# Kernel optimization log

Measured on AMD Instinct MI355X. Metric: run time of the kernel, lower is better.

The kernel has to match this reference:

```python
import jax, jax.numpy as jnp
import numpy as np

EOS_ID = 2
PAD_ID = 0


def setup_inputs() -> dict:
    key = jax.random.key(0)
    ks = jax.random.split(key, 10)
    B, E, H, V, T = 64, 512, 512, 32000, 20
    features = jax.random.normal(ks[0], (B, E), dtype=jnp.float32)
    captions = jax.random.randint(ks[1], (B, T), 0, V)            # unused in policy branch
    lengths = jax.random.randint(ks[2], (B,), 1, T + 1)
    lengths = lengths.at[0].set(T)                                 # make max(lengths) == 20 deterministic
    # parameters (match torch init scales roughly)
    embed_W = jax.random.uniform(ks[3], (V, E), jnp.float32, -0.1, 0.1)
    s = 1.0 / np.sqrt(H)
    W_ih = jax.random.uniform(ks[4], (4 * H, E), jnp.float32, -s, s)
    W_hh = jax.random.uniform(ks[5], (4 * H, H), jnp.float32, -s, s)
    b_ih = jax.random.uniform(ks[6], (4 * H,), jnp.float32, -s, s)
    b_hh = jax.random.uniform(ks[7], (4 * H,), jnp.float32, -s, s)
    linear_W = jax.random.uniform(ks[8], (V, H), jnp.float32, -0.1, 0.1)
    linear_b = jnp.zeros((V,), jnp.float32)
    return {"features": features, "captions": captions, "lengths": lengths,
            "use_policy": 1, "embed_W": embed_W, "W_ih": W_ih, "W_hh": W_hh,
            "b_ih": b_ih, "b_hh": b_hh, "linear_W": linear_W, "linear_b": linear_b}


def _lstm_cell(x, h, c, W_ih, W_hh, b_ih, b_hh):
    # PyTorch gate order: i, f, g, o
    gates = x @ W_ih.T + b_ih + h @ W_hh.T + b_hh        # [B, 4H]
    i, f, g, o = jnp.split(gates, 4, axis=-1)
    i, f, o = jax.nn.sigmoid(i), jax.nn.sigmoid(f), jax.nn.sigmoid(o)
    g = jnp.tanh(g)
    c = f * c + i * g
    h = o * jnp.tanh(c)
    return h, c


def reference(features, captions, lengths, use_policy, embed_W, W_ih, W_hh,
              b_ih, b_hh, linear_W, linear_b):
    # LSTM decode with categorical sampling, stopping per-example at EOS (id 2)
    # and padding remaining steps with id 0 / log_prob 0. The original loops
    # over batch and time with batch-size-1 kernels; here we batch + lax.scan.
    B, H = features.shape[0], W_hh.shape[1]
    T = int(jnp.max(lengths))                            # concrete at trace setup
    step_keys = jax.random.split(jax.random.key(42), T)

    def step(carry, key_t):
        h, c, x, done = carry
        h, c = _lstm_cell(x, h, c, W_ih, W_hh, b_ih, b_hh)
        logits = h @ linear_W.T + linear_b               # [B, V]
        logp = jax.nn.log_softmax(logits, axis=-1)
        tok = jax.random.categorical(key_t, logits)      # [B] int32
        lp = jnp.take_along_axis(logp, tok[:, None], axis=1)[:, 0]
        ids_rec = jnp.where(done, PAD_ID, tok)
        lp_rec = jnp.where(done, 0.0, lp)
        done = done | ((tok == EOS_ID) & ~done)          # EOS token itself is recorded
        x = embed_W[tok]                                 # next-step input embedding
        return (h, c, x, done), (ids_rec, lp_rec)

    init = (jnp.zeros((B, H), features.dtype), jnp.zeros((B, H), features.dtype),
            features, jnp.zeros((B,), bool))
    _, (ids, logps) = jax.lax.scan(step, init, step_keys)
    sampled_ids = jnp.transpose(ids)                     # [B, T]
    saved_log_probs = jnp.transpose(logps)               # [B, T]
    return sampled_ids, saved_log_probs
```

## Files before the change

### kernel.cpp

```cpp
#include <hip/hip_runtime.h>
#include <hip/hip_bf16.h>
#include <stdint.h>
#include <float.h>

#define BB 64
#define EE 512
#define HH 512
#define VV 32000
#define TT 20
#define INV2048 0.00048828125f

typedef _Float16 f16x8 __attribute__((ext_vector_type(8)));
typedef float f32x4 __attribute__((ext_vector_type(4)));

__device__ __host__ __forceinline__ void tf2x32(uint32_t k0, uint32_t k1, uint32_t x0, uint32_t x1,
                                                uint32_t& o0, uint32_t& o1) {
  const uint32_t k2 = k0 ^ k1 ^ 0x1BD11BDAu;
  x0 += k0; x1 += k1;
#define RND(R) { x0 += x1; x1 = (x1 << R) | (x1 >> (32 - R)); x1 ^= x0; }
  RND(13) RND(15) RND(26) RND(6)
  x0 += k1; x1 += k2 + 1u;
  RND(17) RND(29) RND(16) RND(24)
  x0 += k2; x1 += k0 + 2u;
  RND(13) RND(15) RND(26) RND(6)
  x0 += k0; x1 += k1 + 3u;
  RND(17) RND(29) RND(16) RND(24)
  x0 += k1; x1 += k2 + 4u;
  RND(13) RND(15) RND(26) RND(6)
  x0 += k2; x1 += k0 + 5u;
#undef RND
  o0 = x0; o1 = x1;
}

__device__ __forceinline__ float gumbel_for(uint32_t k1t, uint32_t k2t, uint32_t idx) {
  uint32_t o0, o1; tf2x32(k1t, k2t, 0u, idx, o0, o1);
  uint32_t bits = o0 ^ o1;
  uint32_t mant = bits >> 9;
  float f = __uint_as_float(0x3f800000u | mant) - 1.0f;
  float u = mant ? f : 1.1754943508222875e-38f;
  return -logf(-logf(u));
}

struct Part { float bv; int bix; float blog; float m; float s; };

__device__ __forceinline__ void part_combine(Part& P, const Part& Q) {
  if (Q.bv > P.bv || (Q.bv == P.bv && Q.bix < P.bix)) { P.bv = Q.bv; P.bix = Q.bix; P.blog = Q.blog; }
  if (Q.m > P.m) { P.s = P.s * expf(P.m - Q.m) + Q.s; P.m = Q.m; }
  else           { P.s += Q.s * expf(Q.m - P.m); }
}

__global__ __launch_bounds__(256) void k_init(float* __restrict__ hA, float* __restrict__ cT,
                                              int* __restrict__ done) {
  int i = blockIdx.x * 256 + threadIdx.x;
  if (i < HH * BB) { hA[i] = 0.f; cT[i] = 0.f; }
  if (i < BB) done[i] = 0;
}

__global__ __launch_bounds__(256) void k_gates(const float* __restrict__ xin,
                                               const float* __restrict__ hT,
                                               const float* __restrict__ Wih,
                                               const float* __restrict__ Whh,
                                               float* __restrict__ gatesP) {
  const int jt = blockIdx.x;
  const int kc = blockIdx.y;
  const int tx = threadIdx.x;
  __shared__ float a[64][64];
  __shared__ float wj[64][68];
  const int bi = (tx & 15) * 4;
  const int ji = (tx >> 4) * 4;
  float acc[4][4] = {};
  const float* Wsrc = (kc < 4) ? Wih : Whh;
  for (int s = 0; s < 2; ++s) {
    const int kg = kc * 128 + s * 64;
    if (kc < 4) {
      #pragma unroll
      for (int r = 0; r < 4; ++r) {
        int fi = r * 256 + tx;
        int b = fi >> 4, k4 = (fi & 15) * 4;
        const float4 v = *(const float4*)(xin + b * EE + kg + k4);
        a[k4 + 0][b] = v.x; a[k4 + 1][b] = v.y; a[k4 + 2][b] = v.z; a[k4 + 3][b] = v.w;
      }
    } else {
      #pragma unroll
      for (int r = 0; r < 4; ++r) {
        int fi = r * 256 + tx;
        int row = fi >> 4, c4 = (fi & 15) * 4;
        *(float4*)(&a[row][c4]) = *(const float4*)(hT + (kg - 512 + row) * BB + c4);
      }
    }
    const int kcol = kg & 511;
    #pragma unroll
    for (int r = 0; r < 4; ++r) {
      int fi = r * 256 + tx;
      int j = fi >> 4, k4 = (fi & 15) * 4;
      const float4 v = *(const float4*)(Wsrc + (size_t)(jt * 64 + j) * EE + kcol + k4);
      wj[k4 + 0][j] = v.x; wj[k4 + 1][j] = v.y; wj[k4 + 2][j] = v.z; wj[k4 + 3][j] = v.w;
    }
    __syncthreads();
    #pragma unroll 8
    for (int kk = 0; kk < 64; ++kk) {
      const float4 av = *(const float4*)(&a[kk][bi]);
      const float4 wv = *(const float4*)(&wj[kk][ji]);
      const float avx[4] = {av.x, av.y, av.z, av.w};
      const float wvx[4] = {wv.x, wv.y, wv.z, wv.w};
      #pragma unroll
      for (int jj = 0; jj < 4; ++jj)
        #pragma unroll
        for (int bb = 0; bb < 4; ++bb)
          acc[jj][bb] = fmaf(wvx[jj], avx[bb], acc[jj][bb]);
    }
    __syncthreads();
  }
  #pragma unroll
  for (int jj = 0; jj < 4; ++jj) {
    float4 o = make_float4(acc[jj][0], acc[jj][1], acc[jj][2], acc[jj][3]);
    *(float4*)(gatesP + ((size_t)kc * 2048 + jt * 64 + ji + jj) * BB + bi) = o;
  }
}

__global__ __launch_bounds__(256) void k_lstm_update(const float* __restrict__ gatesP,
                                                     const float* __restrict__ b_ih,
                                                     const float* __restrict__ b_hh,
                                                     float* __restrict__ cT,
                                                     float* __restrict__ hT) {
  const int blk = blockIdx.x;
  const int tx = threadIdx.x;
  const int b = tx & 63;
  const int dk = tx >> 6;
  #pragma unroll
  for (int r = 0; r < 2; ++r) {
    const int k = blk * 8 + dk + r * 4;
    float g[4];
    #pragma unroll
    for (int gi = 0; gi < 4; ++gi) {
      const int j = gi * 512 + k;
      float s = 0.f;
      #pragma unroll
      for (int kc = 0; kc < 8; ++kc) s += gatesP[((size_t)kc * 2048 + j) * BB + b];
      g[gi] = s + b_ih[j] + b_hh[j];
    }
    const float ig = 1.f / (1.f + expf(-g[0]));
    const float fg = 1.f / (1.f + expf(-g[1]));
    const float gg = tanhf(g[2]);
    const float og = 1.f / (1.f + expf(-g[3]));
    const float c = fg * cT[k * BB + b] + ig * gg;
    cT[k * BB + b] = c;
    hT[k * BB + b] = og * tanhf(c);
  }
}

__global__ __launch_bounds__(256) void k_lstm_update_frag(const float* __restrict__ gatesP,
                                                          const float* __restrict__ b_ih,
                                                          const float* __restrict__ b_hh,
                                                          float* __restrict__ cT,
                                                          float* __restrict__ hT,
                                                          _Float16* __restrict__ hfh,
                                                          _Float16* __restrict__ hfl) {
  const int blk = blockIdx.x;
  const int tx = threadIdx.x;
  const int b = tx & 63;
  const int dk = tx >> 6;
  #pragma unroll
  for (int r = 0; r < 2; ++r) {
    const int k = blk * 8 + dk + r * 4;
    float g[4];
    #pragma unroll
    for (int gi = 0; gi < 4; ++gi) {
      const int j = gi * 512 + k;
      float s = 0.f;
      #pragma unroll
      for (int kc = 0; kc < 8; ++kc) s += gatesP[((size_t)kc * 2048 + j) * BB + b];
      g[gi] = s + b_ih[j] + b_hh[j];
    }
    const float ig = 1.f / (1.f + expf(-g[0]));
    const float fg = 1.f / (1.f + expf(-g[1]));
    const float gg = tanhf(g[2]);
    const float og = 1.f / (1.f + expf(-g[3]));
    const float c = fg * cT[k * BB + b] + ig * gg;
    cT[k * BB + b] = c;
    const float h = og * tanhf(c);
    hT[k * BB + b] = h;
    const _Float16 hh = (_Float16)h;
    const _Float16 hl = (_Float16)((h - (float)hh) * 2048.0f);
    const int cc = k >> 5, kr = k & 31;
    const int lane = (kr >> 3) * 16 + (b & 15), j = kr & 7, nb = b >> 4;
    const int idx = ((cc * 4 + nb) * 64 + lane) * 8 + j;
    hfh[idx] = hh; hfl[idx] = hl;
  }
}

__global__ __launch_bounds__(256) void k_convW2(const float* __restrict__ LW,
                                                _Float16* __restrict__ Wh,
                                                _Float16* __restrict__ Wl) {
  const int bv = blockIdx.x, bk = blockIdx.y;
  const int tx = threadIdx.x;
  __shared__ float lds[64][65];
  #pragma unroll
  for (int r = 0; r < 4; ++r) {
    const int fi = r * 256 + tx;
    const int vl = fi >> 4, k4 = (fi & 15) * 4;
    const float4 v = *(const float4*)(LW + (size_t)(bv * 64 + vl) * HH + bk * 64 + k4);
    lds[vl][k4] = v.x; lds[vl][k4 + 1] = v.y; lds[vl][k4 + 2] = v.z; lds[vl][k4 + 3] = v.w;
  }
  __syncthreads();
  #pragma unroll
  for (int r = 0; r < 2; ++r) {
    const int u = r * 256 + tx;
    const int frag = u >> 6;
    const int vbl = frag >> 1, cl = frag & 1;
    const int lane = u & 63;
    const int m = lane & 15, lh = lane >> 4;
    f16x8 hi, lo;
    #pragma unroll
    for (int j = 0; j < 8; ++j) {
      const float f = lds[vbl * 16 + m][cl * 32 + lh * 8 + j];
      const _Float16 h = (_Float16)f;
      hi[j] = h;
      lo[j] = (_Float16)((f - (float)h) * 2048.0f);
    }
    const size_t o = (((size_t)(bv * 4 + vbl) * 16 + (bk * 2 + cl)) * 64 + lane) * 8;
    *(f16x8*)(Wh + o) = hi;
    *(f16x8*)(Wl + o) = lo;
  }
}

__global__ __launch_bounds__(256) void k_logits4(const f16x8* __restrict__ Wh,
                                                 const f16x8* __restrict__ Wl,
                                                 const f16x8* __restrict__ hfh,
                                                 const f16x8* __restrict__ hfl,
                                                 const float* __restrict__ lb,
                                                 uint32_t k1t, uint32_t k2t,
                                                 float4* __restrict__ pf4,
                                                 int* __restrict__ pidx) {
  const int wv = threadIdx.x >> 6;
  const int vt = blockIdx.x * 4 + wv;
  const int lane = threadIdx.x & 63;
  __shared__ float red[4][64][5];
  const f32x4 zero = {0.f, 0.f, 0.f, 0.f};
  f32x4 aH[4]  = {zero, zero, zero, zero};
  f32x4 aM1[4] = {zero, zero, zero, zero};
  f32x4 aM2[4] = {zero, zero, zero, zero};
  const size_t wbase = (size_t)vt * 16 * 64 + lane;
  f16x8 whC = Wh[wbase], wlC = Wl[wbase];
  #pragma unroll 4
  for (int c = 0; c < 16; ++c) {
    f16x8 whN, wlN;
    if (c < 15) { whN = Wh[wbase + (c + 1) * 64]; wlN = Wl[wbase + (c + 1) * 64]; }
    #pragma unroll
    for (int nb = 0; nb < 4; ++nb) {
      const f16x8 bh = hfh[(c * 4 + nb) * 64 + lane];
      const f16x8 bl = hfl[(c * 4 + nb) * 64 + lane];
      aH[nb]  = __builtin_amdgcn_mfma_f32_16x16x32_f16(whC, bh, aH[nb], 0, 0, 0);
      aM1[nb] = __builtin_amdgcn_mfma_f32_16x16x32_f16(whC, bl, aM1[nb], 0, 0, 0);
      aM2[nb] = __builtin_amdgcn_mfma_f32_16x16x32_f16(wlC, bh, aM2[nb], 0, 0, 0);
    }
    whC = whN; wlC = wlN;
  }
  const int v0 = vt * 16 + ((lane >> 4) << 2);
  const float4 bias = *(const float4*)(lb + v0);
  const float bb4[4] = {bias.x, bias.y, bias.z, bias.w};
  Part P[4];
  #pragma unroll
  for (int nb = 0; nb < 4; ++nb) {
    const int b = nb * 16 + (lane & 15);
    float lg = aH[nb][0] + (aM1[nb][0] + aM2[nb][0]) * INV2048 + bb4[0];
    Part p;
    p.bv = lg + gumbel_for(k1t, k2t, (uint32_t)(b * VV + v0));
    p.bix = v0; p.blog = lg; p.m = lg; p.s = 1.0f;
    #pragma unroll
    for (int reg = 1; reg < 4; ++reg) {
      float lg2 = aH[nb][reg] + (aM1[nb][reg] + aM2[nb][reg]) * INV2048 + bb4[reg];
      float pe = lg2 + gumbel_for(k1t, k2t, (uint32_t)(b * VV + v0 + reg));
      if (pe > p.bv) { p.bv = pe; p.bix = v0 + reg; p.blog = lg2; }
      if (lg2 > p.m) { p.s = p.s * expf(p.m - lg2) + 1.f; p.m = lg2; }
      else           { p.s += expf(lg2 - p.m); }
    }
    P[nb] = p;
  }
  #pragma unroll
  for (int msk = 16; msk <= 32; msk <<= 1) {
    #pragma unroll
    for (int nb = 0; nb < 4; ++nb) {
      Part Q;
      Q.bv   = __shfl_xor(P[nb].bv, msk, 64);
      Q.bix  = __shfl_xor(P[nb].bix, msk, 64);
      Q.blog = __shfl_xor(P[nb].blog, msk, 64);
      Q.m    = __shfl_xor(P[nb].m, msk, 64);
      Q.s    = __shfl_xor(P[nb].s, msk, 64);
      part_combine(P[nb], Q);
    }
  }
  if (lane < 16) {
    #pragma unroll
    for (int nb = 0; nb < 4; ++nb) {
      const int b = nb * 16 + lane;
      red[wv][b][0] = P[nb].bv; red[wv][b][1] = __int_as_float(P[nb].bix);
      red[wv][b][2] = P[nb].blog; red[wv][b][3] = P[nb].m; red[wv][b][4] = P[nb].s;
    }
  }
  __syncthreads();
  if (threadIdx.x < 64) {
    const int b = threadIdx.x;
    Part Pc;
    Pc.bv = red[0][b][0]; Pc.bix = __float_as_int(red[0][b][1]); Pc.blog = red[0][b][2];
    Pc.m = red[0][b][3]; Pc.s = red[0][b][4];
    #pragma unroll
    for (int w = 1; w < 4; ++w) {
      Part Q;
      Q.bv = red[w][b][0]; Q.bix = __float_as_int(red[w][b][1]); Q.blog = red[w][b][2];
      Q.m = red[w][b][3]; Q.s = red[w][b][4];
      part_combine(Pc, Q);
    }
    pf4[(size_t)blockIdx.x * BB + b] = make_float4(Pc.bv, Pc.blog, Pc.m, Pc.s);
    pidx[blockIdx.x * BB + b] = Pc.bix;
  }
}

__global__ __launch_bounds__(128) void k_logits2(const float* __restrict__ hT,
                                                 const float* __restrict__ LW,
                                                 const float* __restrict__ lb,
                                                 uint32_t k1t, uint32_t k2t,
                                                 float4* __restrict__ pf4,
                                                 int* __restrict__ pidx) {
  const int vt = blockIdx.x;
  const int tx = threadIdx.x;
  __shared__ float lds[5120];
  float* wTs = lds;
  const int vthr = tx & 15;
  const int bthr = tx >> 4;
  const int vi = vthr * 2;
  const int bi = bthr * 8;
  const int vq = tx >> 4;
  const int ks = tx & 15;
  float acc[2][8] = {};
  for (int kt = 0; kt < 8; ++kt) {
    const int kg = kt * 64;
    #pragma unroll
    for (int s = 0; s < 4; ++s) {
      const int kk = ks + 16 * s;
      const size_t rb = (size_t)(vt * 32 + 4 * vq) * HH + kg + kk;
      float w0 = LW[rb];
      float w1 = LW[rb + HH];
      float w2 = LW[rb + 2 * HH];
      float w3 = LW[rb + 3 * HH];
      const int ph = (4 * vq) ^ (4 * (kk & 7));
      *(float4*)&wTs[kk * 32 + ph] = make_float4(w0, w1, w2, w3);
    }
    __syncthreads();
    #pragma unroll 4
    for (int kk = 0; kk < 64; ++kk) {
      const float* hrow = hT + (size_t)(kg + kk) * BB;
      const float4 h0 = *(const float4*)(hrow + bi);
      const float4 h1 = *(const float4*)(hrow + bi + 4);
      const float2 wv = *(const float2*)&wTs[kk * 32 + (vi ^ (4 * (kk & 7)))];
      acc[0][0] = fmaf(wv.x, h0.x, acc[0][0]); acc[0][1] = fmaf(wv.x, h0.y, acc[0][1]);
      acc[0][2] = fmaf(wv.x, h0.z, acc[0][2]); acc[0][3] = fmaf(wv.x, h0.w, acc[0][3]);
      acc[0][4] = fmaf(wv.x, h1.x, acc[0][4]); acc[0][5] = fmaf(wv.x, h1.y, acc[0][5]);
      acc[0][6] = fmaf(wv.x, h1.z, acc[0][6]); acc[0][7] = fmaf(wv.x, h1.w, acc[0][7]);
      acc[1][0] = fmaf(wv.y, h0.x, acc[1][0]); acc[1][1] = fmaf(wv.y, h0.y, acc[1][1]);
      acc[1][2] = fmaf(wv.y, h0.z, acc[1][2]); acc[1][3] = fmaf(wv.y, h0.w, acc[1][3]);
      acc[1][4] = fmaf(wv.y, h1.x, acc[1][4]); acc[1][5] = fmaf(wv.y, h1.y, acc[1][5]);
      acc[1][6] = fmaf(wv.y, h1.z, acc[1][6]); acc[1][7] = fmaf(wv.y, h1.w, acc[1][7]);
    }
    __syncthreads();
  }
  const int v0g = vt * 32 + vi;
  const float bias0 = lb[v0g];
  const float bias1 = lb[v0g + 1];
  float* red = lds;
  #pragma unroll
  for (int bb = 0; bb < 8; ++bb) {
    const int b = bi + bb;
    const float lg0 = acc[0][bb] + bias0;
    const float lg1 = acc[1][bb] + bias1;
    Part p;
    p.bv = lg0 + gumbel_for(k1t, k2t, (uint32_t)(b * VV + v0g));
    p.bix = v0g; p.blog = lg0;
    const float pe1 = lg1 + gumbel_for(k1t, k2t, (uint32_t)(b * VV + v0g + 1));
    if (pe1 > p.bv) { p.bv = pe1; p.bix = v0g + 1; p.blog = lg1; }
    if (lg0 >= lg1) { p.m = lg0; p.s = 1.f + expf(lg1 - lg0); }
    else            { p.m = lg1; p.s = 1.f + expf(lg0 - lg1); }
    const int slot = (b * 16 + vthr) * 5;
    red[slot + 0] = p.bv; red[slot + 1] = __int_as_float(p.bix); red[slot + 2] = p.blog;
    red[slot + 3] = p.m;  red[slot + 4] = p.s;
  }
  __syncthreads();
  if (tx < 64) {
    const int b = tx;
    Part P;
    { const int s0 = (b * 16) * 5;
      P.bv = red[s0]; P.bix = __float_as_int(red[s0 + 1]); P.blog = red[s0 + 2];
      P.m = red[s0 + 3]; P.s = red[s0 + 4]; }
    #pragma unroll
    for (int c = 1; c < 16; ++c) {
      const int s0 = (b * 16 + c) * 5;
      Part Q; Q.bv = red[s0]; Q.bix = __float_as_int(red[s0 + 1]); Q.blog = red[s0 + 2];
      Q.m = red[s0 + 3]; Q.s = red[s0 + 4];
      part_combine(P, Q);
    }
    pf4[(size_t)vt * BB + b] = make_float4(P.bv, P.blog, P.m, P.s);
    pidx[vt * BB + b] = P.bix;
  }
}

__global__ __launch_bounds__(256) void k_sample2(const float4* __restrict__ pf4,
                                                 const int* __restrict__ pidx,
                                                 const float* __restrict__ embW,
                                                 int* __restrict__ done,
                                                 float* __restrict__ x,
                                                 float* __restrict__ out,
                                                 int step, int nvt) {
  const int b = blockIdx.x;
  const int tx = threadIdx.x;
  __shared__ float red[256 * 5];
  __shared__ int stok;
  Part p; p.bv = -FLT_MAX; p.bix = 0x7fffffff; p.blog = 0.f; p.m = -FLT_MAX; p.s = 0.f;
  for (int vt = tx; vt < nvt; vt += 256) {
    float4 q = pf4[(size_t)vt * BB + b];
    Part Q; Q.bv = q.x; Q.blog = q.y; Q.m = q.z; Q.s = q.w; Q.bix = pidx[vt * BB + b];
    part_combine(p, Q);
  }
  red[tx * 5 + 0] = p.bv; red[tx * 5 + 1] = __int_as_float(p.bix); red[tx * 5 + 2] = p.blog;
  red[tx * 5 + 3] = p.m;  red[tx * 5 + 4] = p.s;
  __syncthreads();
  for (int st = 128; st > 0; st >>= 1) {
    if (tx < st) {
      const int s0 = tx * 5, s1 = (tx + st) * 5;
      Part P, Q;
      P.bv = red[s0]; P.bix = __float_as_int(red[s0 + 1]); P.blog = red[s0 + 2]; P.m = red[s0 + 3]; P.s = red[s0 + 4];
      Q.bv = red[s1]; Q.bix = __float_as_int(red[s1 + 1]); Q.blog = red[s1 + 2]; Q.m = red[s1 + 3]; Q.s = red[s1 + 4];
      part_combine(P, Q);
      red[s0] = P.bv; red[s0 + 1] = __int_as_float(P.bix); red[s0 + 2] = P.blog; red[s0 + 3] = P.m; red[s0 + 4] = P.s;
    }
    __syncthreads();
  }
  if (tx == 0) {
    const int tok = __float_as_int(red[1]);
    const float blog = red[2], M = red[3], S = red[4];
    const float lp = blog - (M + logf(S));
    const int dn = done[b];
    out[b * TT + step] = dn ? 0.0f : (float)tok;
    out[BB * TT + b * TT + step] = dn ? 0.0f : lp;
    done[b] = dn | (tok == 2);
    stok = tok;
  }
  __syncthreads();
  const int tok = stok;
  for (int e = tx; e < EE; e += 256) x[b * EE + e] = embW[(size_t)tok * EE + e];
}

extern "C" void kernel_launch(void* const* d_in, const int* in_sizes, int n_in,
                              void* d_out, int out_size, void* d_ws, size_t ws_size,
                              hipStream_t stream) {
  const float* features = (const float*)d_in[0];
  const float* embW     = (const float*)d_in[4];
  const float* Wih      = (const float*)d_in[5];
  const float* Whh      = (const float*)d_in[6];
  const float* bih      = (const float*)d_in[7];
  const float* bhh      = (const float*)d_in[8];
  const float* LW       = (const float*)d_in[9];
  const float* lb       = (const float*)d_in[10];
  float* out = (float*)d_out;

  uint32_t keys[TT][2];
  for (int t = 0; t < TT; ++t) tf2x32(0u, 42u, 0u, (uint32_t)t, keys[t][0], keys[t][1]);

  float* ws = (float*)d_ws;
  float* hA = ws;
  float* hB = ws + 32768;
  float* cT = ws + 65536;
  float* x  = ws + 98304;

  if (ws_size >= (size_t)73000000) {
    float*  gatesP = ws + 131072;
    float4* pf4    = (float4*)(ws + 1179648);
    int*    pidx   = (int*)(ws + 1691648);
    int*    done   = (int*)(ws + 1819648);
    _Float16* hfh  = (_Float16*)(ws + 1819712);
    _Float16* hfl  = (_Float16*)(ws + 1836096);
    _Float16* Whi  = (_Float16*)(ws + 1852480);
    _Float16* Wlo  = (_Float16*)(ws + 10044480);

    k_convW2<<<dim3(500, 8), dim3(256), 0, stream>>>(LW, Whi, Wlo);
    k_init<<<dim3(128), dim3(256), 0, stream>>>(hA, cT, done);
    const float* hin = hA;
    float* hout = hB;
    for (int t = 0; t < TT; ++t) {
      const float* xin = (t == 0) ? features : x;
      k_gates<<<dim3(32, 8), dim3(256), 0, stream>>>(xin, hin, Wih, Whh, gatesP);
      k_lstm_update_frag<<<dim3(64), dim3(256), 0, stream>>>(gatesP, bih, bhh, cT, hout, hfh, hfl);
      k_logits4<<<dim3(500), dim3(256), 0, stream>>>((const f16x8*)Whi, (const f16x8*)Wlo,
                                                     (const f16x8*)hfh, (const f16x8*)hfl,
                                                     lb, keys[t][0], keys[t][1], pf4, pidx);
      k_sample2<<<dim3(64), dim3(256), 0, stream>>>(pf4, pidx, embW, done, x, out, t, 500);
      const float* tmp = hout; hout = (float*)hin; hin = tmp;
    }
  } else {
    float*  gatesP = ws + 131072;
    float4* pf4    = (float4*)(ws + 131072 + 1048576);
    int*    pidx   = (int*)(ws + 131072 + 1048576 + 256000);
    int*    done   = (int*)(ws + 131072 + 1048576 + 256000 + 64000);

    k_init<<<dim3(128), dim3(256), 0, stream>>>(hA, cT, done);
    const float* hin = hA;
    float* hout = hB;
    for (int t = 0; t < TT; ++t) {
      const float* xin = (t == 0) ? features : x;
      k_gates<<<dim3(32, 8), dim3(256), 0, stream>>>(xin, hin, Wih, Whh, gatesP);
      k_lstm_update<<<dim3(64), dim3(256), 0, stream>>>(gatesP, bih, bhh, cT, hout);
      k_logits2<<<dim3(1000), dim3(128), 0, stream>>>(hout, LW, lb, keys[t][0], keys[t][1], pf4, pidx);
      k_sample2<<<dim3(64), dim3(256), 0, stream>>>(pf4, pidx, embW, done, x, out, t, 1000);
      const float* tmp = hout; hout = (float*)hin; hin = tmp;
    }
  }
}
```

Before: 935.3 us.

## Fuse embedding gather into gates kernel and deepen logits prefetch pipeline

The sampling kernel now writes only the sampled token ids, and the gate GEMM kernel gathers embedding rows directly by token id. This removes the intermediate x buffer write and read on every step. The logits MFMA loop now prefetches weight fragments four chunks ahead and double-buffers the hidden-state fragments in registers, which is meant to hide global load latency. The cost is higher register pressure in the logits kernel and scattered row reads of the embedding table inside the gates kernel.

Result: slower. 1.051 ms (+12.4%).

```diff
diff --git a/kernel.cpp b/kernel.cpp
--- a/kernel.cpp
+++ b/kernel.cpp
@@ -56,20 +56,61 @@
   if (i < BB) done[i] = 0;
 }
 
-__global__ __launch_bounds__(256) void k_gates(const float* __restrict__ xin,
-                                               const float* __restrict__ hT,
-                                               const float* __restrict__ Wih,
-                                               const float* __restrict__ Whh,
-                                               float* __restrict__ gatesP) {
+__global__ __launch_bounds__(256) void k_convW2(const float* __restrict__ LW,
+                                                _Float16* __restrict__ Wh,
+                                                _Float16* __restrict__ Wl) {
+  const int bv = blockIdx.x, bk = blockIdx.y;
+  const int tx = threadIdx.x;
+  __shared__ float lds[64][65];
+  #pragma unroll
+  for (int r = 0; r < 4; ++r) {
+    const int fi = r * 256 + tx;
+    const int vl = fi >> 4, k4 = (fi & 15) * 4;
+    const float4 v = *(const float4*)(LW + (size_t)(bv * 64 + vl) * HH + bk * 64 + k4);
+    lds[vl][k4] = v.x; lds[vl][k4 + 1] = v.y; lds[vl][k4 + 2] = v.z; lds[vl][k4 + 3] = v.w;
+  }
+  __syncthreads();
+  #pragma unroll
+  for (int r = 0; r < 2; ++r) {
+    const int u = r * 256 + tx;
+    const int frag = u >> 6;
+    const int vbl = frag >> 1, cl = frag & 1;
+    const int lane = u & 63;
+    const int m = lane & 15, lh = lane >> 4;
+    f16x8 hi, lo;
+    #pragma unroll
+    for (int j = 0; j < 8; ++j) {
+      const float f = lds[vbl * 16 + m][cl * 32 + lh * 8 + j];
+      const _Float16 h = (_Float16)f;
+      hi[j] = h;
+      lo[j] = (_Float16)((f - (float)h) * 2048.0f);
+    }
+    const size_t o = (((size_t)(bv * 4 + vbl) * 16 + (bk * 2 + cl)) * 64 + lane) * 8;
+    *(f16x8*)(Wh + o) = hi;
+    *(f16x8*)(Wl + o) = lo;
+  }
+}
+
+__global__ __launch_bounds__(256) void k_gates2(const float* __restrict__ xin,
+                                                const float* __restrict__ embW,
+                                                const int* __restrict__ tok,
+                                                int use_tok,
+                                                const float* __restrict__ hT,
+                                                const float* __restrict__ Wih,
+                                                const float* __restrict__ Whh,
+                                                float* __restrict__ gatesP) {
   const int jt = blockIdx.x;
   const int kc = blockIdx.y;
   const int tx = threadIdx.x;
   __shared__ float a[64][64];
   __shared__ float wj[64][68];
+  __shared__ int ltok[64];
+  if (tx < 64) ltok[tx] = use_tok ? tok[tx] : 0;
   const int bi = (tx & 15) * 4;
   const int ji = (tx >> 4) * 4;
   float acc[4][4] = {};
   const float* Wsrc = (kc < 4) ? Wih : Whh;
+  __syncthreads();
   for (int s = 0; s < 2; ++s) {
     const int kg = kc * 128 + s * 64;
     if (kc < 4) {
@@ -77,7 +118,8 @@
       for (int r = 0; r < 4; ++r) {
         int fi = r * 256 + tx;
         int b = fi >> 4, k4 = (fi & 15) * 4;
-        const float4 v = *(const float4*)(xin + b * EE + kg + k4);
+        const float* rowsrc = use_tok ? (embW + (size_t)ltok[b] * EE) : (xin + (size_t)b * EE);
+        const float4 v = *(const float4*)(rowsrc + kg + k4);
         a[k4 + 0][b] = v.x; a[k4 + 1][b] = v.y; a[k4 + 2][b] = v.z; a[k4 + 3][b] = v.w;
       }
     } else {
@@ -115,37 +157,6 @@
   for (int jj = 0; jj < 4; ++jj) {
     float4 o = make_float4(acc[jj][0], acc[jj][1], acc[jj][2], acc[jj][3]);
     *(float4*)(gatesP + ((size_t)kc * 2048 + jt * 64 + ji + jj) * BB + bi) = o;
-  }
-}
-
-__global__ __launch_bounds__(256) void k_lstm_update(const float* __restrict__ gatesP,
-                                                     const float* __restrict__ b_ih,
-                                                     const float* __restrict__ b_hh,
-                                                     float* __restrict__ cT,
-                                                     float* __restrict__ hT) {
-  const int blk = blockIdx.x;
-  const int tx = threadIdx.x;
-  const int b = tx & 63;
-  const int dk = tx >> 6;
-  #pragma unroll
-  for (int r = 0; r < 2; ++r) {
-    const int k = blk * 8 + dk + r * 4;
-    float g[4];
-    #pragma unroll
-    for (int gi = 0; gi < 4; ++gi) {
-      const int j = gi * 512 + k;
-      float s = 0.f;
-      #pragma unroll
-      for (int kc = 0; kc < 8; ++kc) s += gatesP[((size_t)kc * 2048 + j) * BB + b];
-      g[gi] = s + b_ih[j] + b_hh[j];
-    }
-    const float ig = 1.f / (1.f + expf(-g[0]));
-    const float fg = 1.f / (1.f + expf(-g[1]));
-    const float gg = tanhf(g[2]);
-    const float og = 1.f / (1.f + expf(-g[3]));
-    const float c = fg * cT[k * BB + b] + ig * gg;
-    cT[k * BB + b] = c;
-    hT[k * BB + b] = og * tanhf(c);
   }
 }
 
@@ -189,42 +200,7 @@
   }
 }
 
-__global__ __launch_bounds__(256) void k_convW2(const float* __restrict__ LW,
-                                                _Float16* __restrict__ Wh,
-                                                _Float16* __restrict__ Wl) {
-  const int bv = blockIdx.x, bk = blockIdx.y;
-  const int tx = threadIdx.x;
-  __shared__ float lds[64][65];
-  #pragma unroll
-  for (int r = 0; r < 4; ++r) {
-    const int fi = r * 256 + tx;
-    const int vl = fi >> 4, k4 = (fi & 15) * 4;
-    const float4 v = *(const float4*)(LW + (size_t)(bv * 64 + vl) * HH + bk * 64 + k4);
-    lds[vl][k4] = v.x; lds[vl][k4 + 1] = v.y; lds[vl][k4 + 2] = v.z; lds[vl][k4 + 3] = v.w;
-  }
-  __syncthreads();
-  #pragma unroll
-  for (int r = 0; r < 2; ++r) {
-    const int u = r * 256 + tx;
-    const int frag = u >> 6;
-    const int vbl = frag >> 1, cl = frag & 1;
-    const int lane = u & 63;
-    const int m = lane & 15, lh = lane >> 4;
-    f16x8 hi, lo;
-    #pragma unroll
-    for (int j = 0; j < 8; ++j) {
-      const float f = lds[vbl * 16 + m][cl * 32 + lh * 8 + j];
-      const _Float16 h = (_Float16)f;
-      hi[j] = h;
-      lo[j] = (_Float16)((f - (float)h) * 2048.0f);
-    }
-    const size_t o = (((size_t)(bv * 4 + vbl) * 16 + (bk * 2 + cl)) * 64 + lane) * 8;
-    *(f16x8*)(Wh + o) = hi;
-    *(f16x8*)(Wl + o) = lo;
-  }
-}
-
-__global__ __launch_bounds__(256) void k_logits4(const f16x8* __restrict__ Wh,
+__global__ __launch_bounds__(256) void k_logits5(const f16x8* __restrict__ Wh,
                                                  const f16x8* __restrict__ Wl,
                                                  const f16x8* __restrict__ hfh,
                                                  const f16x8* __restrict__ hfl,
@@ -241,20 +217,32 @@
   f32x4 aM1[4] = {zero, zero, zero, zero};
   f32x4 aM2[4] = {zero, zero, zero, zero};
   const size_t wbase = (size_t)vt * 16 * 64 + lane;
-  f16x8 whC = Wh[wbase], wlC = Wl[wbase];
-  #pragma unroll 4
+  f16x8 whR[4], wlR[4];
+  #pragma unroll
+  for (int i = 0; i < 4; ++i) { whR[i] = Wh[wbase + i * 64]; wlR[i] = Wl[wbase + i * 64]; }
+  f16x8 bhN[4], blN[4];
+  #pragma unroll
+  for (int nb = 0; nb < 4; ++nb) { bhN[nb] = hfh[nb * 64 + lane]; blN[nb] = hfl[nb * 64 + lane]; }
+  #pragma unroll
   for (int c = 0; c < 16; ++c) {
-    f16x8 whN, wlN;
-    if (c < 15) { whN = Wh[wbase + (c + 1) * 64]; wlN = Wl[wbase + (c + 1) * 64]; }
+    const f16x8 whC = whR[c & 3], wlC = wlR[c & 3];
+    if (c + 4 < 16) { whR[c & 3] = Wh[wbase + (c + 4) * 64]; wlR[c & 3] = Wl[wbase + (c + 4) * 64]; }
+    f16x8 bhC[4], blC[4];
+    #pragma unroll
+    for (int nb = 0; nb < 4; ++nb) { bhC[nb] = bhN[nb]; blC[nb] = blN[nb]; }
+    if (c < 15) {
+      #pragma unroll
+      for (int nb = 0; nb < 4; ++nb) {
+        bhN[nb] = hfh[((c + 1) * 4 + nb) * 64 + lane];
+        blN[nb] = hfl[((c + 1) * 4 + nb) * 64 + lane];
+      }
+    }
     #pragma unroll
     for (int nb = 0; nb < 4; ++nb) {
-      const f16x8 bh = hfh[(c * 4 + nb) * 64 + lane];
-      const f16x8 bl = hfl[(c * 4 + nb) * 64 + lane];
-      aH[nb]  = __builtin_amdgcn_mfma_f32_16x16x32_f16(whC, bh, aH[nb], 0, 0, 0);
-      aM1[nb] = __builtin_amdgcn_mfma_f32_16x16x32_f16(whC, bl, aM1[nb], 0, 0, 0);
-      aM2[nb] = __builtin_amdgcn_mfma_f32_16x16x32_f16(wlC, bh, aM2[nb], 0, 0, 0);
-    }
-    whC = whN; wlC = wlN;
+      aH[nb]  = __builtin_amdgcn_mfma_f32_16x16x32_f16(whC, bhC[nb], aH[nb], 0, 0, 0);
+      aM1[nb] = __builtin_amdgcn_mfma_f32_16x16x32_f16(whC, blC[nb], aM1[nb], 0, 0, 0);
+      aM2[nb] = __builtin_amdgcn_mfma_f32_16x16x32_f16(wlC, bhC[nb], aM2[nb], 0, 0, 0);
+    }
   }
   const int v0 = vt * 16 + ((lane >> 4) << 2);
   const float4 bias = *(const float4*)(lb + v0);
@@ -313,6 +301,78 @@
     }
     pf4[(size_t)blockIdx.x * BB + b] = make_float4(Pc.bv, Pc.blog, Pc.m, Pc.s);
     pidx[blockIdx.x * BB + b] = Pc.bix;
+  }
+}
+
+__global__ __launch_bounds__(256) void k_sample4(const float4* __restrict__ pf4,
+                                                 const int* __restrict__ pidx,
+                                                 int* __restrict__ done,
+                                                 int* __restrict__ tokb,
+                                                 float* __restrict__ out,
+                                                 int step) {
+  const int b = blockIdx.x;
+  const int tx = threadIdx.x;
+  __shared__ float red[256 * 5];
+  Part p; p.bv = -FLT_MAX; p.bix = 0x7fffffff; p.blog = 0.f; p.m = -FLT_MAX; p.s = 0.f;
+  for (int vt = tx; vt < 500; vt += 256) {
+    float4 q = pf4[(size_t)vt * BB + b];
+    Part Q; Q.bv = q.x; Q.blog = q.y; Q.m = q.z; Q.s = q.w; Q.bix = pidx[vt * BB + b];
+    part_combine(p, Q);
+  }
+  red[tx * 5 + 0] = p.bv; red[tx * 5 + 1] = __int_as_float(p.bix); red[tx * 5 + 2] = p.blog;
+  red[tx * 5 + 3] = p.m;  red[tx * 5 + 4] = p.s;
+  __syncthreads();
+  for (int st = 128; st > 0; st >>= 1) {
+    if (tx < st) {
+      const int s0 = tx * 5, s1 = (tx + st) * 5;
+      Part P, Q;
+      P.bv = red[s0]; P.bix = __float_as_int(red[s0 + 1]); P.blog = red[s0 + 2]; P.m = red[s0 + 3]; P.s = red[s0 + 4];
+      Q.bv = red[s1]; Q.bix = __float_as_int(red[s1 + 1]); Q.blog = red[s1 + 2]; Q.m = red[s1 + 3]; Q.s = red[s1 + 4];
+      part_combine(P, Q);
+      red[s0] = P.bv; red[s0 + 1] = __int_as_float(P.bix); red[s0 + 2] = P.blog; red[s0 + 3] = P.m; red[s0 + 4] = P.s;
+    }
+    __syncthreads();
+  }
+  if (tx == 0) {
+    const int tok = __float_as_int(red[1]);
+    const float blog = red[2], M = red[3], S = red[4];
+    const float lp = blog - (M + logf(S));
+    const int dn = done[b];
+    out[b * TT + step] = dn ? 0.0f : (float)tok;
+    out[BB * TT + b * TT + step] = dn ? 0.0f : lp;
+    done[b] = dn | (tok == 2);
+    tokb[b] = tok;
+  }
+}
+
+__global__ __launch_bounds__(256) void k_lstm_update(const float* __restrict__ gatesP,
+                                                     const float* __restrict__ b_ih,
+                                                     const float* __restrict__ b_hh,
+                                                     float* __restrict__ cT,
+                                                     float* __restrict__ hT) {
+  const int blk = blockIdx.x;
+  const int tx = threadIdx.x;
+  const int b = tx & 63;
+  const int dk = tx >> 6;
+  #pragma unroll
+  for (int r = 0; r < 2; ++r) {
+    const int k = blk * 8 + dk + r * 4;
+    float g[4];
+    #pragma unroll
+    for (int gi = 0; gi < 4; ++gi) {
+      const int j = gi * 512 + k;
+      float s = 0.f;
+      #pragma unroll
+      for (int kc = 0; kc < 8; ++kc) s += gatesP[((size_t)kc * 2048 + j) * BB + b];
+      g[gi] = s + b_ih[j] + b_hh[j];
+    }
+    const float ig = 1.f / (1.f + expf(-g[0]));
+    const float fg = 1.f / (1.f + expf(-g[1]));
+    const float gg = tanhf(g[2]);
+    const float og = 1.f / (1.f + expf(-g[3]));
+    const float c = fg * cT[k * BB + b] + ig * gg;
+    cT[k * BB + b] = c;
+    hT[k * BB + b] = og * tanhf(c);
   }
 }
 
@@ -466,12 +526,12 @@
   for (int t = 0; t < TT; ++t) tf2x32(0u, 42u, 0u, (uint32_t)t, keys[t][0], keys[t][1]);
 
   float* ws = (float*)d_ws;
-  float* hA = ws;
-  float* hB = ws + 32768;
-  float* cT = ws + 65536;
-  float* x  = ws + 98304;
 
   if (ws_size >= (size_t)73000000) {
+    float* hA = ws;
+    float* hB = ws + 32768;
+    float* cT = ws + 65536;
+    int*   tokb = (int*)(ws + 98304);
     float*  gatesP = ws + 131072;
     float4* pf4    = (float4*)(ws + 1179648);
     int*    pidx   = (int*)(ws + 1691648);
@@ -486,16 +546,20 @@
     const float* hin = hA;
     float* hout = hB;
     for (int t = 0; t < TT; ++t) {
-      const float* xin = (t == 0) ? features : x;
-      k_gates<<<dim3(32, 8), dim3(256), 0, stream>>>(xin, hin, Wih, Whh, gatesP);
+      k_gates2<<<dim3(32, 8), dim3(256), 0, stream>>>(features, embW, tokb, (t > 0) ? 1 : 0,
+                                                      hin, Wih, Whh, gatesP);
       k_lstm_update_frag<<<dim3(64), dim3(256), 0, stream>>>(gatesP, bih, bhh, cT, hout, hfh, hfl);
-      k_logits4<<<dim3(500), dim3(256), 0, stream>>>((const f16x8*)Whi, (const f16x8*)Wlo,
+      k_logits5<<<dim3(500), dim3(256), 0, stream>>>((const f16x8*)Whi, (const f16x8*)Wlo,
                                                      (const f16x8*)hfh, (const f16x8*)hfl,
                                                      lb, keys[t][0], keys[t][1], pf4, pidx);
-      k_sample2<<<dim3(64), dim3(256), 0, stream>>>(pf4, pidx, embW, done, x, out, t, 500);
+      k_sample4<<<dim3(64), dim3(256), 0, stream>>>(pf4, pidx, done, tokb, out, t);
       const float* tmp = hout; hout = (float*)hin; hin = tmp;
     }
   } else {
+    float* hA = ws;
+    float* hB = ws + 32768;
+    float* cT = ws + 65536;
+    float* x  = ws + 98304;
     float*  gatesP = ws + 131072;
     float4* pf4    = (float4*)(ws + 131072 + 1048576);
     int*    pidx   = (int*)(ws + 131072 + 1048576 + 256000);
@@ -506,7 +570,8 @@
     float* hout = hB;
     for (int t = 0; t < TT; ++t) {
       const float* xin = (t == 0) ? features : x;
-      k_gates<<<dim3(32, 8), dim3(256), 0, stream>>>(xin, hin, Wih, Whh, gatesP);
+      k_gates2<<<dim3(32, 8), dim3(256), 0, stream>>>(xin, embW, done , 0,
+                                                      hin, Wih, Whh, gatesP);
       k_lstm_update<<<dim3(64), dim3(256), 0, stream>>>(gatesP, bih, bhh, cT, hout);
       k_logits2<<<dim3(1000), dim3(128), 0, stream>>>(hout, LW, lb, keys[t][0], keys[t][1], pf4, pidx);
       k_sample2<<<dim3(64), dim3(256), 0, stream>>>(pf4, pidx, embW, done, x, out, t, 1000);
```
